# Kernel tuning notes

Measured on AMD Instinct MI355X. Metric: run time of the kernel, lower is better.

## Reference

```python
import jax, jax.numpy as jnp
import numpy as np

B, F = 4096, 128          # batch, num fields
L = 3                     # att_layer_num
H1, H2 = 256, 128         # dnn_hidden_units


def setup_inputs() -> dict:
    key = jax.random.key(0)
    ks = jax.random.split(key, 10)
    X = jax.random.normal(ks[0], (B, F), dtype=jnp.float32)
    # InteractingLayer params: embedding_size=1, head_num=1 -> (1,1) matrices, std=0.05
    wq = jax.random.normal(ks[1], (L, 1, 1), dtype=jnp.float32) * 0.05
    wk = jax.random.normal(ks[2], (L, 1, 1), dtype=jnp.float32) * 0.05
    wv = jax.random.normal(ks[3], (L, 1, 1), dtype=jnp.float32) * 0.05
    wr = jax.random.normal(ks[4], (L, 1, 1), dtype=jnp.float32) * 0.05
    # DNN: Linear(F->H1), Linear(H1->H2) with init_std=1e-4 weights, zero-ish bias
    W1 = jax.random.normal(ks[5], (F, H1), dtype=jnp.float32) * 1e-4
    b1 = jnp.zeros((H1,), dtype=jnp.float32)
    W2 = jax.random.normal(ks[6], (H1, H2), dtype=jnp.float32) * 1e-4
    b2 = jnp.zeros((H2,), dtype=jnp.float32)
    # dnn_linear: Linear(H2 -> 1, bias=False)
    Wf = jax.random.normal(ks[7], (H2, 1), dtype=jnp.float32) * 0.05
    return {"X": X, "wq": wq, "wk": wk, "wv": wv, "wr": wr,
            "W1": W1, "b1": b1, "W2": W2, "b2": b2, "Wf": Wf}


def _interact(x, wq, wk, wv, wr):
    # x: (B, F, 1); w*: (1, 1). head_num=1, att_embedding_size=1, no scaling.
    q = jnp.einsum('bfe,ed->bfd', x, wq)
    k = jnp.einsum('bfe,ed->bfd', x, wk)
    v = jnp.einsum('bfe,ed->bfd', x, wv)
    scores = jax.nn.softmax(jnp.einsum('bfd,bgd->bfg', q, k), axis=-1)  # (B,F,F)
    out = jnp.einsum('bfg,bgd->bfd', scores, v)
    out = out + jnp.einsum('bfe,ed->bfd', x, wr)  # use_res residual
    return jax.nn.relu(out)


def reference(X, wq, wk, wv, wr, W1, b1, W2, b2, Wf):
    att = X[..., None]  # (B, F, 1)
    for i in range(L):
        att = _interact(att, wq[i], wk[i], wv[i], wr[i])
    h = att.reshape(att.shape[0], -1)          # (B, F)
    h = jax.nn.relu(h @ W1 + b1)               # (B, H1)
    h = jax.nn.relu(h @ W2 + b2)               # (B, H2)
    return h @ Wf                              # (B, 1)
```

## Files before the change

### kernel.cpp

```cpp
#include <hip/hip_runtime.h>
#include <hip/hip_bf16.h>


#define FDIM 128
#define NLAYER 3
#define H1 256
#define H2 128
#define RPB 8

__global__ __launch_bounds__(FDIM) void autoint_attn_kernel(
    const float* __restrict__ X,
    const float* __restrict__ wq, const float* __restrict__ wk,
    const float* __restrict__ wv, const float* __restrict__ wr,
    float* __restrict__ att)
{
    __shared__ float sx[FDIM];
    const int b = blockIdx.x;
    const int f = threadIdx.x;

    float xf = X[b * FDIM + f];
    sx[f] = xf;
    __syncthreads();

    #pragma unroll
    for (int l = 0; l < NLAYER; ++l) {
        const float c  = wq[l] * wk[l] * 1.4426950408889634f;
        const float vv = wv[l];
        const float rr = wr[l];

        const float a = c * xf;
        float den = 0.f, num = 0.f;

        #pragma unroll 2
        for (int g = 0; g < FDIM; g += 4) {
            float4 xg = *reinterpret_cast<const float4*>(&sx[g]);
            float e0 = __builtin_amdgcn_exp2f(a * xg.x);
            float e1 = __builtin_amdgcn_exp2f(a * xg.y);
            float e2 = __builtin_amdgcn_exp2f(a * xg.z);
            float e3 = __builtin_amdgcn_exp2f(a * xg.w);
            den += (e0 + e1) + (e2 + e3);
            num = fmaf(e0, xg.x, num);
            num = fmaf(e1, xg.y, num);
            num = fmaf(e2, xg.z, num);
            num = fmaf(e3, xg.w, num);
        }

        float o = fmaf(rr, xf, vv * num / den);
        o = fmaxf(o, 0.f);

        __syncthreads();
        sx[f] = o;
        xf = o;
        __syncthreads();
    }

    att[b * FDIM + f] = xf;
}

__global__ __launch_bounds__(256) void autoint_dnn_kernel(
    const float* __restrict__ att,
    const float* __restrict__ W1, const float* __restrict__ b1,
    const float* __restrict__ W2, const float* __restrict__ b2,
    const float* __restrict__ Wf,
    float* __restrict__ out)
{
    __shared__ float sh[RPB][FDIM];
    __shared__ float sh1[RPB][H1];
    __shared__ float red[RPB][2];

    const int tid = threadIdx.x;
    const int b0  = blockIdx.x * RPB;

    #pragma unroll
    for (int i = tid; i < RPB * FDIM; i += 256)
        sh[i >> 7][i & (FDIM - 1)] = att[b0 * FDIM + i];
    __syncthreads();

    {
        float acc[RPB];
        const float bb = b1[tid];
        #pragma unroll
        for (int r = 0; r < RPB; ++r) acc[r] = bb;

        #pragma unroll 4
        for (int i = 0; i < FDIM; ++i) {
            const float w = W1[i * H1 + tid];
            #pragma unroll
            for (int r = 0; r < RPB; ++r)
                acc[r] = fmaf(sh[r][i], w, acc[r]);
        }
        #pragma unroll
        for (int r = 0; r < RPB; ++r)
            sh1[r][tid] = fmaxf(acc[r], 0.f);
    }
    __syncthreads();

    {
        const int k  = tid & (H2 - 1);
        const int rb = (tid >> 7) * 4;
        float acc[4];
        const float bb = b2[k];
        #pragma unroll
        for (int r = 0; r < 4; ++r) acc[r] = bb;

        #pragma unroll 4
        for (int j = 0; j < H1; ++j) {
            const float w = W2[j * H2 + k];
            #pragma unroll
            for (int r = 0; r < 4; ++r)
                acc[r] = fmaf(sh1[rb + r][j], w, acc[r]);
        }

        const float wf = Wf[k];
        float p[4];
        #pragma unroll
        for (int r = 0; r < 4; ++r)
            p[r] = fmaxf(acc[r], 0.f) * wf;

        #pragma unroll
        for (int off = 32; off >= 1; off >>= 1) {
            #pragma unroll
            for (int r = 0; r < 4; ++r)
                p[r] += __shfl_down(p[r], off, 64);
        }
        const int lane = tid & 63;
        const int wave = tid >> 6;
        if (lane == 0) {
            #pragma unroll
            for (int r = 0; r < 4; ++r)
                red[rb + r][wave & 1] = p[r];
        }
    }
    __syncthreads();

    if (tid < RPB)
        out[b0 + tid] = red[tid][0] + red[tid][1];
}

extern "C" void kernel_launch(void* const* d_in, const int* in_sizes, int n_in,
                              void* d_out, int out_size, void* d_ws, size_t ws_size,
                              hipStream_t stream) {
    const float* X  = (const float*)d_in[0];
    const float* wq = (const float*)d_in[1];
    const float* wk = (const float*)d_in[2];
    const float* wv = (const float*)d_in[3];
    const float* wr = (const float*)d_in[4];
    const float* W1 = (const float*)d_in[5];
    const float* b1 = (const float*)d_in[6];
    const float* W2 = (const float*)d_in[7];
    const float* b2 = (const float*)d_in[8];
    const float* Wf = (const float*)d_in[9];
    float* out = (float*)d_out;

    const int B = in_sizes[0] / FDIM;
    float* att = (float*)d_ws;

    autoint_attn_kernel<<<dim3(B), dim3(FDIM), 0, stream>>>(
        X, wq, wk, wv, wr, att);
    autoint_dnn_kernel<<<dim3(B / RPB), dim3(256), 0, stream>>>(
        att, W1, b1, W2, b2, Wf, out);
}
```

Measured before the change: 130.5 us.

## Fuse attention and DNN into one kernel with split-K partial sums

```diff
diff --git a/kernel.cpp b/kernel.cpp
--- a/kernel.cpp
+++ b/kernel.cpp
@@ -4,22 +4,31 @@
 
 #define FDIM 128
 #define NLAYER 3
+#define RPB 8
 #define H1 256
 #define H2 128
-#define RPB 8
 
-__global__ __launch_bounds__(FDIM) void autoint_attn_kernel(
+__global__ __launch_bounds__(1024) void autoint_fused(
     const float* __restrict__ X,
     const float* __restrict__ wq, const float* __restrict__ wk,
     const float* __restrict__ wv, const float* __restrict__ wr,
-    float* __restrict__ att)
+    const float* __restrict__ W1, const float* __restrict__ b1,
+    const float* __restrict__ W2, const float* __restrict__ b2,
+    const float* __restrict__ Wf,
+    float* __restrict__ out)
 {
-    __shared__ float sx[FDIM];
-    const int b = blockIdx.x;
-    const int f = threadIdx.x;
+    __shared__ float sx[RPB][FDIM];
+    __shared__ float sh1[RPB][H1];
+    __shared__ float part[8192];
+    __shared__ float red[RPB][2];
 
-    float xf = X[b * FDIM + f];
-    sx[f] = xf;
+    const int tid = threadIdx.x;
+    const int b0  = blockIdx.x * RPB;
+
+    const int r = tid >> 7;
+    const int f = tid & 127;
+    float xf = X[(b0 + r) * FDIM + f];
+    sx[r][f] = xf;
     __syncthreads();
 
     #pragma unroll
@@ -31,9 +40,9 @@
         const float a = c * xf;
         float den = 0.f, num = 0.f;
 
-        #pragma unroll 2
+        #pragma unroll 4
         for (int g = 0; g < FDIM; g += 4) {
-            float4 xg = *reinterpret_cast<const float4*>(&sx[g]);
+            float4 xg = *reinterpret_cast<const float4*>(&sx[r][g]);
             float e0 = __builtin_amdgcn_exp2f(a * xg.x);
             float e1 = __builtin_amdgcn_exp2f(a * xg.y);
             float e2 = __builtin_amdgcn_exp2f(a * xg.z);
@@ -45,91 +54,80 @@
             num = fmaf(e3, xg.w, num);
         }
 
-        float o = fmaf(rr, xf, vv * num / den);
-        o = fmaxf(o, 0.f);
-
+        float o = fmaxf(fmaf(rr, xf, vv * num / den), 0.f);
         __syncthreads();
-        sx[f] = o;
+        sx[r][f] = o;
         xf = o;
         __syncthreads();
     }
 
-    att[b * FDIM + f] = xf;
-}
+    {
+        const int j  = tid & 255;
+        const int kq = tid >> 8;
+        float acc[RPB];
+        #pragma unroll
+        for (int q = 0; q < RPB; ++q) acc[q] = 0.f;
 
-__global__ __launch_bounds__(256) void autoint_dnn_kernel(
-    const float* __restrict__ att,
-    const float* __restrict__ W1, const float* __restrict__ b1,
-    const float* __restrict__ W2, const float* __restrict__ b2,
-    const float* __restrict__ Wf,
-    float* __restrict__ out)
-{
-    __shared__ float sh[RPB][FDIM];
-    __shared__ float sh1[RPB][H1];
-    __shared__ float red[RPB][2];
-
-    const int tid = threadIdx.x;
-    const int b0  = blockIdx.x * RPB;
-
-    #pragma unroll
-    for (int i = tid; i < RPB * FDIM; i += 256)
-        sh[i >> 7][i & (FDIM - 1)] = att[b0 * FDIM + i];
-    __syncthreads();
-
-    {
-        float acc[RPB];
-        const float bb = b1[tid];
-        #pragma unroll
-        for (int r = 0; r < RPB; ++r) acc[r] = bb;
-
-        #pragma unroll 4
-        for (int i = 0; i < FDIM; ++i) {
-            const float w = W1[i * H1 + tid];
+        const int i0 = kq * 32;
+        #pragma unroll 8
+        for (int ii = 0; ii < 32; ++ii) {
+            const int i = i0 + ii;
+            const float w = W1[i * H1 + j];
             #pragma unroll
-            for (int r = 0; r < RPB; ++r)
-                acc[r] = fmaf(sh[r][i], w, acc[r]);
+            for (int q = 0; q < RPB; ++q)
+                acc[q] = fmaf(sx[q][i], w, acc[q]);
         }
         #pragma unroll
-        for (int r = 0; r < RPB; ++r)
-            sh1[r][tid] = fmaxf(acc[r], 0.f);
+        for (int q = 0; q < RPB; ++q)
+            part[kq * 2048 + q * 256 + j] = acc[q];
+    }
+    __syncthreads();
+    {
+        #pragma unroll
+        for (int idx = tid; idx < RPB * H1; idx += 1024) {
+            const int q = idx >> 8, j = idx & 255;
+            float s = b1[j] + ((part[idx] + part[2048 + idx]) +
+                               (part[4096 + idx] + part[6144 + idx]));
+            sh1[q][j] = fmaxf(s, 0.f);
+        }
     }
     __syncthreads();
 
     {
-        const int k  = tid & (H2 - 1);
-        const int rb = (tid >> 7) * 4;
-        float acc[4];
-        const float bb = b2[k];
+        const int k  = tid & 127;
+        const int kq = tid >> 7;
+        float acc[RPB];
         #pragma unroll
-        for (int r = 0; r < 4; ++r) acc[r] = bb;
+        for (int q = 0; q < RPB; ++q) acc[q] = 0.f;
 
-        #pragma unroll 4
-        for (int j = 0; j < H1; ++j) {
+        const int j0 = kq * 32;
+        #pragma unroll 8
+        for (int jj = 0; jj < 32; ++jj) {
+            const int j = j0 + jj;
             const float w = W2[j * H2 + k];
             #pragma unroll
-            for (int r = 0; r < 4; ++r)
-                acc[r] = fmaf(sh1[rb + r][j], w, acc[r]);
+            for (int q = 0; q < RPB; ++q)
+                acc[q] = fmaf(sh1[q][j], w, acc[q]);
         }
-
-        const float wf = Wf[k];
-        float p[4];
         #pragma unroll
-        for (int r = 0; r < 4; ++r)
-            p[r] = fmaxf(acc[r], 0.f) * wf;
+        for (int q = 0; q < RPB; ++q)
+            part[kq * 1024 + q * 128 + k] = acc[q];
+    }
+    __syncthreads();
+    {
+        const int r2 = tid >> 7;
+        const int k  = tid & 127;
+        float s = b2[k];
+        #pragma unroll
+        for (int q = 0; q < 8; ++q)
+            s += part[q * 1024 + r2 * 128 + k];
+        float p = fmaxf(s, 0.f) * Wf[k];
 
         #pragma unroll
-        for (int off = 32; off >= 1; off >>= 1) {
-            #pragma unroll
-            for (int r = 0; r < 4; ++r)
-                p[r] += __shfl_down(p[r], off, 64);
-        }
-        const int lane = tid & 63;
-        const int wave = tid >> 6;
-        if (lane == 0) {
-            #pragma unroll
-            for (int r = 0; r < 4; ++r)
-                red[rb + r][wave & 1] = p[r];
-        }
+        for (int off = 32; off >= 1; off >>= 1)
+            p += __shfl_down(p, off, 64);
+        if ((tid & 63) == 0)
+            red[r2][(tid >> 6) & 1] = p;
     }
     __syncthreads();
 
@@ -153,10 +151,6 @@
     float* out = (float*)d_out;
 
     const int B = in_sizes[0] / FDIM;
-    float* att = (float*)d_ws;
-
-    autoint_attn_kernel<<<dim3(B), dim3(FDIM), 0, stream>>>(
-        X, wq, wk, wv, wr, att);
-    autoint_dnn_kernel<<<dim3(B / RPB), dim3(256), 0, stream>>>(
-        att, W1, b1, W2, b2, Wf, out);
+    autoint_fused<<<dim3(B / RPB), dim3(1024), 0, stream>>>(
+        X, wq, wk, wv, wr, W1, b1, W2, b2, Wf, out);
 }
```

Result: no change. 128.4 us (-1.6%).
